# Kernel tuning notes

Measured on AMD Instinct MI355X. Metric: run time of the kernel, lower is better.

The kernel has to match this reference:

```python
import jax, jax.numpy as jnp
import numpy as np

LATENT = 16
HID = 512
N_CLASSES = 10
STYLE = 64
B = 8192


def _he(key, shape, fan_in):
    return jax.random.normal(key, shape, dtype=jnp.float32) * jnp.sqrt(2.0 / fan_in)


def setup_inputs() -> dict:
    key = jax.random.key(0)
    ks = jax.random.split(key, 20)
    inp = {}
    inp['z'] = jax.random.normal(ks[0], (B, LATENT), dtype=jnp.float32)
    inp['y'] = jax.random.randint(ks[1], (B,), 0, N_CLASSES)
    inp['sw0'] = _he(ks[2], (LATENT, HID), LATENT)
    inp['sb0'] = jnp.zeros((HID,), jnp.float32)
    inp['sw1'] = _he(ks[3], (HID, HID), HID)
    inp['sb1'] = jnp.zeros((HID,), jnp.float32)
    inp['sw2'] = _he(ks[4], (HID, HID), HID)
    inp['sb2'] = jnp.zeros((HID,), jnp.float32)
    inp['sw3'] = _he(ks[5], (HID, HID), HID)
    inp['sb3'] = jnp.zeros((HID,), jnp.float32)
    # unshared per-class experts stacked on leading class axis C
    inp['uw0'] = _he(ks[6], (N_CLASSES, HID, HID), HID)
    inp['ub0'] = jnp.zeros((N_CLASSES, HID), jnp.float32)
    inp['uw1'] = _he(ks[7], (N_CLASSES, HID, HID), HID)
    inp['ub1'] = jnp.zeros((N_CLASSES, HID), jnp.float32)
    inp['uw2'] = _he(ks[8], (N_CLASSES, HID, HID), HID)
    inp['ub2'] = jnp.zeros((N_CLASSES, HID), jnp.float32)
    inp['uw3'] = _he(ks[9], (N_CLASSES, HID, STYLE), HID)
    inp['ub3'] = jnp.zeros((N_CLASSES, STYLE), jnp.float32)
    return inp


def reference(z, y, sw0, sb0, sw1, sb1, sw2, sb2, sw3, sb3,
              uw0, ub0, uw1, ub1, uw2, ub2, uw3, ub3):
    # shared trunk: 4 Linear+ReLU
    h = jax.nn.relu(z @ sw0 + sb0)
    h = jax.nn.relu(h @ sw1 + sb1)
    h = jax.nn.relu(h @ sw2 + sb2)
    h = jax.nn.relu(h @ sw3 + sb3)          # [B, H]
    # all per-class expert branches (matches original dense computation)
    o = jax.nn.relu(jnp.einsum('bd,cde->bce', h, uw0) + ub0)   # [B, C, H]
    o = jax.nn.relu(jnp.einsum('bcd,cde->bce', o, uw1) + ub1)
    o = jax.nn.relu(jnp.einsum('bcd,cde->bce', o, uw2) + ub2)
    out = jnp.einsum('bcd,cds->bcs', o, uw3) + ub3             # [B, C, S], no ReLU
    # gather the branch matching each sample's class
    s = out[jnp.arange(out.shape[0]), y]                        # [B, S]
    return s
```

## Files before the change

### kernel.cpp

```cpp
#include <hip/hip_runtime.h>

#define B_SAMPLES 8192
#define HID       512
#define NCLS      10
#define STYLE_D   64
#define LATENT_D  16

#define BM 128
#define BN 64
#define BK 64
#define MAXT    (B_SAMPLES/BM + NCLS)
#define MAXROWS (B_SAMPLES + NCLS*BM)

typedef short v8s __attribute__((ext_vector_type(8)));
typedef float v4f __attribute__((ext_vector_type(4)));

__device__ __forceinline__ short f2bf(float f) {
    union { float f; unsigned u; } x; x.f = f;
    unsigned r = x.u + 0x7fffu + ((x.u >> 16) & 1u);
    return (short)(r >> 16);
}

__device__ __forceinline__ void gload16(const short* g, short* l) {
    __builtin_amdgcn_global_load_lds(
        (const __attribute__((address_space(1))) void*)g,
        (__attribute__((address_space(3))) void*)l, 16, 0, 0);
}

__device__ __forceinline__ int kswz(int row, int k) {
    return (k & ~63) + ((((k >> 3) & 7) ^ (row & 7)) << 3) + (k & 7);
}
__device__ __forceinline__ int cswz(int key, int n0, int c) {
    return n0 + ((((c >> 3) ^ key) & 7) << 3) + (c & 7);
}

__global__ void build_groups(const int* __restrict__ y, int* __restrict__ tclass,
                             int* __restrict__ trow0, int* __restrict__ order,
                             int* __restrict__ rank) {
    __shared__ int cnt[NCLS], cur[NCLS];
    int t = threadIdx.x;
    if (t < NCLS) cnt[t] = 0;
    __syncthreads();
    for (int b = t; b < B_SAMPLES; b += 1024) atomicAdd(&cnt[y[b]], 1);
    __syncthreads();
    if (t == 0) {
        int off = 0, tt = 0;
        for (int c = 0; c < NCLS; ++c) {
            cur[c] = off;
            int nt = (cnt[c] + BM - 1) / BM;
            for (int j = 0; j < nt; ++j) { tclass[tt] = c; trow0[tt] = off + j * BM; ++tt; }
            off += nt * BM;
        }
        for (int u = tt; u < MAXT; ++u) { tclass[u] = -1; trow0[u] = 0; }
    }
    __syncthreads();
    for (int i = t; i < MAXROWS; i += 1024) order[i] = -1;
    __syncthreads();
    for (int b = t; b < B_SAMPLES; b += 1024) {
        int c = y[b];
        int p = atomicAdd(&cur[c], 1);
        order[p] = b;
        rank[b] = p;
    }
}

__global__ void transpose_mega(const float* __restrict__ z,
                               const float* __restrict__ sw0, const float* __restrict__ sw1,
                               const float* __restrict__ sw2, const float* __restrict__ sw3,
                               const float* __restrict__ uw0, const float* __restrict__ uw1,
                               const float* __restrict__ uw2, const float* __restrict__ uw3,
                               short* __restrict__ zb,
                               short* __restrict__ wt0, short* __restrict__ wt1,
                               short* __restrict__ wt2, short* __restrict__ wt3,
                               short* __restrict__ wtu0, short* __restrict__ wtu1,
                               short* __restrict__ wtu2, short* __restrict__ wtu3) {
    __shared__ float tile[32][33];
    int zz = blockIdx.z;
    int tx = threadIdx.x, ty = threadIdx.y;
    if (zz == 35) {
        int t = ty * 32 + tx;
        int base = (blockIdx.y * 20 + blockIdx.x) * 256 + t;
        for (int i = base; i < B_SAMPLES * 64; i += 320 * 256) {
            int b = i >> 6, k = i & 63;
            zb[b * 64 + kswz(b, k)] =
                f2bf(k < LATENT_D ? z[(size_t)b * LATENT_D + k] : 0.f);
        }
        return;
    }
    if (zz == 34) {
        if (blockIdx.x >= 16 || blockIdx.y >= 2) return;
        int n0 = blockIdx.x * 32, k0 = blockIdx.y * 32;
        #pragma unroll
        for (int j = 0; j < 32; j += 8) {
            int k = k0 + ty + j;
            tile[ty + j][tx] = (k < LATENT_D) ? sw0[(size_t)k * HID + n0 + tx] : 0.f;
        }
        __syncthreads();
        #pragma unroll
        for (int j = 0; j < 32; j += 8) {
            int n = n0 + ty + j, k = k0 + tx;
            wt0[n * 64 + kswz(n, k)] = f2bf(tile[tx][ty + j]);
        }
        return;
    }
    if (zz == 33) {
        int cls = blockIdx.x >> 1;
        int n0 = (blockIdx.x & 1) * 32, k0 = blockIdx.y * 32;
        const float* s = uw3  + (size_t)cls * HID * STYLE_D;
        short*       d = wtu3 + (size_t)cls * STYLE_D * HID;
        #pragma unroll
        for (int j = 0; j < 32; j += 8)
            tile[ty + j][tx] = s[(size_t)(k0 + ty + j) * STYLE_D + n0 + tx];
        __syncthreads();
        #pragma unroll
        for (int j = 0; j < 32; j += 8) {
            int n = n0 + ty + j, k = k0 + tx;
            d[(size_t)n * HID + kswz(n, k)] = f2bf(tile[tx][ty + j]);
        }
        return;
    }
    if (blockIdx.x >= 16) return;
    const float* s; short* d;
    if      (zz == 0) { s = sw1; d = wt1; }
    else if (zz == 1) { s = sw2; d = wt2; }
    else if (zz == 2) { s = sw3; d = wt3; }
    else if (zz < 13) { size_t o = (size_t)(zz - 3)  * HID * HID; s = uw0 + o; d = wtu0 + o; }
    else if (zz < 23) { size_t o = (size_t)(zz - 13) * HID * HID; s = uw1 + o; d = wtu1 + o; }
    else              { size_t o = (size_t)(zz - 23) * HID * HID; s = uw2 + o; d = wtu2 + o; }
    int n0 = blockIdx.x * 32, k0 = blockIdx.y * 32;
    #pragma unroll
    for (int j = 0; j < 32; j += 8)
        tile[ty + j][tx] = s[(size_t)(k0 + ty + j) * HID + n0 + tx];
    __syncthreads();
    #pragma unroll
    for (int j = 0; j < 32; j += 8) {
        int n = n0 + ty + j, k = k0 + tx;
        d[(size_t)n * HID + kswz(n, k)] = f2bf(tile[tx][ty + j]);
    }
}

template <int MODE, int NK>
__global__ __launch_bounds__(256, 2) void gemmp(
    const short* __restrict__ A, const short* __restrict__ WT,
    const float* __restrict__ bias, void* __restrict__ Outv,
    const int N, const long wStride, const int biasN,
    const int* __restrict__ aux, const int* __restrict__ tclass,
    const int* __restrict__ trow0) {

    constexpr int K = NK * BK;
    const unsigned gx = gridDim.x;
    const unsigned nwg = gx * gridDim.y;
    unsigned lin = blockIdx.x + gx * blockIdx.y;
    {
        unsigned q = nwg >> 3, r = nwg & 7, xcd = lin & 7, idx = lin >> 3;
        lin = (xcd < r ? xcd * (q + 1) : r * (q + 1) + (xcd - r) * q) + idx;
    }
    const unsigned bx = lin % gx, by = lin / gx;

    int tile = by, cls = 0, row0;
    if (MODE <= 1) {
        row0 = tile * BM;
    } else {
        cls = tclass[tile];
        if (cls < 0) return;
        row0 = trow0[tile];
    }
    const int n0 = bx * BN;
    const short* wt = WT + (size_t)cls * wStride;
    const float* bs = bias + (size_t)cls * biasN;

    __shared__ short As[3][BM * BK];
    __shared__ short Bs[3][BN * BK];

    const int t = threadIdx.x, lane = t & 63, w = t >> 6;
    const int srow = lane >> 3, scol = (lane & 7) * 8;
    const int wr = w >> 1, wc = w & 1;
    const int lrow = lane & 15, lko = lane >> 4;
    const int key = lrow & 7;

    v4f acc[4][2] = {};

    auto stage = [&](int buf, int k0) {
        #pragma unroll
        for (int p = 0; p < 4; ++p) {
            int row = p * 32 + w * 8 + srow;
            gload16(A + (size_t)(row0 + row) * K + k0 + scol, &As[buf][p * 2048 + w * 512]);
        }
        #pragma unroll
        for (int q2 = 0; q2 < 2; ++q2) {
            int row = q2 * 32 + w * 8 + srow;
            gload16(wt + (size_t)(n0 + row) * K + k0 + scol, &Bs[buf][q2 * 2048 + w * 512]);
        }
    };

    stage(0, 0);
    if (NK > 1) stage(1, BK);

    #pragma unroll
    for (int ks = 0; ks < NK; ++ks) {
        const int buf = ks % 3;
        if (ks < NK - 1) asm volatile("s_waitcnt vmcnt(6)" ::: "memory");
        else             asm volatile("s_waitcnt vmcnt(0)" ::: "memory");
        asm volatile("s_barrier" ::: "memory");
        if (ks + 2 < NK) stage((ks + 2) % 3, (ks + 2) * BK);

        __builtin_amdgcn_s_setprio(1);
        #pragma unroll
        for (int kk = 0; kk < 2; ++kk) {
            int ch = ((kk * 4 + lko) ^ key) << 3;
            v8s af[4], bq[2];
            #pragma unroll
            for (int i = 0; i < 4; ++i)
                af[i] = *(const v8s*)&As[buf][(wr * 64 + i * 16 + lrow) * BK + ch];
            #pragma unroll
            for (int j = 0; j < 2; ++j)
                bq[j] = *(const v8s*)&Bs[buf][(wc * 32 + j * 16 + lrow) * BK + ch];
            #pragma unroll
            for (int i = 0; i < 4; ++i)
                #pragma unroll
                for (int j = 0; j < 2; ++j)
                    acc[i][j] = __builtin_amdgcn_mfma_f32_16x16x32_bf16(
                        af[i], bq[j], acc[i][j], 0, 0, 0);
        }
        __builtin_amdgcn_s_setprio(0);
    }

    #pragma unroll
    for (int i = 0; i < 4; ++i)
        #pragma unroll
        for (int j = 0; j < 2; ++j)
            #pragma unroll
            for (int q3 = 0; q3 < 4; ++q3) {
                int rr = wr * 64 + i * 16 + lko * 4 + q3;
                int c = wc * 32 + j * 16 + lrow;
                if (MODE == 3) {
                    int o = aux[row0 + rr];
                    if (o >= 0)
                        ((float*)Outv)[(size_t)o * STYLE_D + n0 + c] = acc[i][j][q3] + bs[n0 + c];
                } else {
                    float v = fmaxf(acc[i][j][q3] + bs[n0 + c], 0.f);
                    int orow = (MODE == 1) ? aux[row0 + rr] : (row0 + rr);
                    ((short*)Outv)[(size_t)orow * N + cswz(orow & 7, n0, c)] = f2bf(v);
                }
            }
}

extern "C" void kernel_launch(void* const* d_in, const int* in_sizes, int n_in,
                              void* d_out, int out_size, void* d_ws, size_t ws_size,
                              hipStream_t stream) {
    const float* z   = (const float*)d_in[0];
    const int*   y   = (const int*)d_in[1];
    const float* sw0 = (const float*)d_in[2];
    const float* sb0 = (const float*)d_in[3];
    const float* sw1 = (const float*)d_in[4];
    const float* sb1 = (const float*)d_in[5];
    const float* sw2 = (const float*)d_in[6];
    const float* sb2 = (const float*)d_in[7];
    const float* sw3 = (const float*)d_in[8];
    const float* sb3 = (const float*)d_in[9];
    const float* uw0 = (const float*)d_in[10];
    const float* ub0 = (const float*)d_in[11];
    const float* uw1 = (const float*)d_in[12];
    const float* ub1 = (const float*)d_in[13];
    const float* uw2 = (const float*)d_in[14];
    const float* ub2 = (const float*)d_in[15];
    const float* uw3 = (const float*)d_in[16];
    const float* ub3 = (const float*)d_in[17];

    char* p = (char*)d_ws;
    auto alloc = [&](size_t bytes) -> char* {
        char* r = p; p += (bytes + 255) & ~(size_t)255; return r;
    };
    int*   tclass = (int*)alloc(MAXT * 4);
    int*   trow0  = (int*)alloc(MAXT * 4);
    int*   order  = (int*)alloc(MAXROWS * 4);
    int*   rank   = (int*)alloc(B_SAMPLES * 4);
    short* zb     = (short*)alloc((size_t)B_SAMPLES * 64 * 2);
    short* wt0    = (short*)alloc((size_t)HID * 64 * 2);
    short* wt1    = (short*)alloc((size_t)HID * HID * 2);
    short* wt2    = (short*)alloc((size_t)HID * HID * 2);
    short* wt3    = (short*)alloc((size_t)HID * HID * 2);
    short* wtu0   = (short*)alloc((size_t)NCLS * HID * HID * 2);
    short* wtu1   = (short*)alloc((size_t)NCLS * HID * HID * 2);
    short* wtu2   = (short*)alloc((size_t)NCLS * HID * HID * 2);
    short* wtu3   = (short*)alloc((size_t)NCLS * STYLE_D * HID * 2);
    short* act0   = (short*)alloc((size_t)MAXROWS * HID * 2);
    short* act1   = (short*)alloc((size_t)MAXROWS * HID * 2);
    short* act2   = (short*)alloc((size_t)MAXROWS * HID * 2);

    build_groups<<<1, 1024, 0, stream>>>(y, tclass, trow0, order, rank);
    dim3 tb(32, 8);
    transpose_mega<<<dim3(20, 16, 36), tb, 0, stream>>>(
        z, sw0, sw1, sw2, sw3, uw0, uw1, uw2, uw3,
        zb, wt0, wt1, wt2, wt3, wtu0, wtu1, wtu2, wtu3);

    gemmp<0, 1><<<dim3(HID / BN, B_SAMPLES / BM), 256, 0, stream>>>(
        zb, wt0, sb0, act0, HID, 0, 0, nullptr, nullptr, nullptr);
    gemmp<0, 8><<<dim3(HID / BN, B_SAMPLES / BM), 256, 0, stream>>>(
        act0, wt1, sb1, act1, HID, 0, 0, nullptr, nullptr, nullptr);
    gemmp<0, 8><<<dim3(HID / BN, B_SAMPLES / BM), 256, 0, stream>>>(
        act1, wt2, sb2, act0, HID, 0, 0, nullptr, nullptr, nullptr);
    gemmp<1, 8><<<dim3(HID / BN, B_SAMPLES / BM), 256, 0, stream>>>(
        act0, wt3, sb3, act2, HID, 0, 0, rank, nullptr, nullptr);

    gemmp<2, 8><<<dim3(HID / BN, MAXT), 256, 0, stream>>>(
        act2, wtu0, ub0, act0, HID, (long)HID * HID, HID, nullptr, tclass, trow0);
    gemmp<2, 8><<<dim3(HID / BN, MAXT), 256, 0, stream>>>(
        act0, wtu1, ub1, act1, HID, (long)HID * HID, HID, nullptr, tclass, trow0);
    gemmp<2, 8><<<dim3(HID / BN, MAXT), 256, 0, stream>>>(
        act1, wtu2, ub2, act0, HID, (long)HID * HID, HID, nullptr, tclass, trow0);
    gemmp<3, 8><<<dim3(1, MAXT), 256, 0, stream>>>(
        act0, wtu3, ub3, d_out, HID, (long)STYLE_D * HID, STYLE_D, order, tclass, trow0);
}
```

Before: 124.9 us.

## Use 8-wave GEMM blocks with double buffering and fuse prep kernels

Each GEMM block now runs 512 threads (8 waves). Each wave computes a 32x32 sub-tile instead of 64x32, and loads are spread across more waves. The 3-stage LDS pipeline with explicit vmcnt waits and setprio is replaced by a simpler 2-stage double buffer synchronized with __syncthreads. The build_groups kernel is folded into the transpose/prep kernel as an extra z-slice to save a launch. The aim is more waves to hide latency, at the cost of less per-wave reuse, a shallower prefetch and heavier barrier traffic.

```diff
diff --git a/kernel.cpp b/kernel.cpp
--- a/kernel.cpp
+++ b/kernel.cpp
@@ -34,51 +34,51 @@
     return n0 + ((((c >> 3) ^ key) & 7) << 3) + (c & 7);
 }
 
-__global__ void build_groups(const int* __restrict__ y, int* __restrict__ tclass,
-                             int* __restrict__ trow0, int* __restrict__ order,
-                             int* __restrict__ rank) {
-    __shared__ int cnt[NCLS], cur[NCLS];
-    int t = threadIdx.x;
-    if (t < NCLS) cnt[t] = 0;
-    __syncthreads();
-    for (int b = t; b < B_SAMPLES; b += 1024) atomicAdd(&cnt[y[b]], 1);
-    __syncthreads();
-    if (t == 0) {
-        int off = 0, tt = 0;
-        for (int c = 0; c < NCLS; ++c) {
-            cur[c] = off;
-            int nt = (cnt[c] + BM - 1) / BM;
-            for (int j = 0; j < nt; ++j) { tclass[tt] = c; trow0[tt] = off + j * BM; ++tt; }
-            off += nt * BM;
-        }
-        for (int u = tt; u < MAXT; ++u) { tclass[u] = -1; trow0[u] = 0; }
-    }
-    __syncthreads();
-    for (int i = t; i < MAXROWS; i += 1024) order[i] = -1;
-    __syncthreads();
-    for (int b = t; b < B_SAMPLES; b += 1024) {
-        int c = y[b];
-        int p = atomicAdd(&cur[c], 1);
-        order[p] = b;
-        rank[b] = p;
-    }
-}
-
-__global__ void transpose_mega(const float* __restrict__ z,
-                               const float* __restrict__ sw0, const float* __restrict__ sw1,
-                               const float* __restrict__ sw2, const float* __restrict__ sw3,
-                               const float* __restrict__ uw0, const float* __restrict__ uw1,
-                               const float* __restrict__ uw2, const float* __restrict__ uw3,
-                               short* __restrict__ zb,
-                               short* __restrict__ wt0, short* __restrict__ wt1,
-                               short* __restrict__ wt2, short* __restrict__ wt3,
-                               short* __restrict__ wtu0, short* __restrict__ wtu1,
-                               short* __restrict__ wtu2, short* __restrict__ wtu3) {
+__global__ void prep_all(const float* __restrict__ z, const int* __restrict__ y,
+                         const float* __restrict__ sw0, const float* __restrict__ sw1,
+                         const float* __restrict__ sw2, const float* __restrict__ sw3,
+                         const float* __restrict__ uw0, const float* __restrict__ uw1,
+                         const float* __restrict__ uw2, const float* __restrict__ uw3,
+                         short* __restrict__ zb,
+                         short* __restrict__ wt0, short* __restrict__ wt1,
+                         short* __restrict__ wt2, short* __restrict__ wt3,
+                         short* __restrict__ wtu0, short* __restrict__ wtu1,
+                         short* __restrict__ wtu2, short* __restrict__ wtu3,
+                         int* __restrict__ tclass, int* __restrict__ trow0,
+                         int* __restrict__ order, int* __restrict__ rank) {
     __shared__ float tile[32][33];
     int zz = blockIdx.z;
     int tx = threadIdx.x, ty = threadIdx.y;
+    int t = ty * 32 + tx;
+    if (zz == 36) {
+        if (blockIdx.x || blockIdx.y) return;
+        __shared__ int cnt[NCLS], cur[NCLS];
+        if (t < NCLS) cnt[t] = 0;
+        __syncthreads();
+        for (int b = t; b < B_SAMPLES; b += 256) atomicAdd(&cnt[y[b]], 1);
+        __syncthreads();
+        if (t == 0) {
+            int off = 0, tt = 0;
+            for (int c = 0; c < NCLS; ++c) {
+                cur[c] = off;
+                int nt = (cnt[c] + BM - 1) / BM;
+                for (int j = 0; j < nt; ++j) { tclass[tt] = c; trow0[tt] = off + j * BM; ++tt; }
+                off += nt * BM;
+            }
+            for (int u = tt; u < MAXT; ++u) { tclass[u] = -1; trow0[u] = 0; }
+        }
+        __syncthreads();
+        for (int i = t; i < MAXROWS; i += 256) order[i] = -1;
+        __syncthreads();
+        for (int b = t; b < B_SAMPLES; b += 256) {
+            int c = y[b];
+            int p = atomicAdd(&cur[c], 1);
+            order[p] = b;
+            rank[b] = p;
+        }
+        return;
+    }
     if (zz == 35) {
-        int t = ty * 32 + tx;
         int base = (blockIdx.y * 20 + blockIdx.x) * 256 + t;
         for (int i = base; i < B_SAMPLES * 64; i += 320 * 256) {
             int b = i >> 6, k = i & 63;
@@ -105,6 +105,7 @@
     }
     if (zz == 33) {
         int cls = blockIdx.x >> 1;
+        if (cls >= NCLS) return;
         int n0 = (blockIdx.x & 1) * 32, k0 = blockIdx.y * 32;
         const float* s = uw3  + (size_t)cls * HID * STYLE_D;
         short*       d = wtu3 + (size_t)cls * STYLE_D * HID;
@@ -140,7 +141,7 @@
 }
 
 template <int MODE, int NK>
-__global__ __launch_bounds__(256, 2) void gemmp(
+__global__ __launch_bounds__(512, 4) void gemm8w(
     const short* __restrict__ A, const short* __restrict__ WT,
     const float* __restrict__ bias, void* __restrict__ Outv,
     const int N, const long wStride, const int biasN,
@@ -169,8 +170,8 @@
     const short* wt = WT + (size_t)cls * wStride;
     const float* bs = bias + (size_t)cls * biasN;
 
-    __shared__ short As[3][BM * BK];
-    __shared__ short Bs[3][BN * BK];
+    __shared__ short As[2][BM * BK];
+    __shared__ short Bs[2][BN * BK];
 
     const int t = threadIdx.x, lane = t & 63, w = t >> 6;
     const int srow = lane >> 3, scol = (lane & 7) * 8;
@@ -178,60 +179,54 @@
     const int lrow = lane & 15, lko = lane >> 4;
     const int key = lrow & 7;
 
-    v4f acc[4][2] = {};
+    v4f acc[2][2] = {};
 
     auto stage = [&](int buf, int k0) {
         #pragma unroll
-        for (int p = 0; p < 4; ++p) {
-            int row = p * 32 + w * 8 + srow;
-            gload16(A + (size_t)(row0 + row) * K + k0 + scol, &As[buf][p * 2048 + w * 512]);
-        }
-        #pragma unroll
-        for (int q2 = 0; q2 < 2; ++q2) {
-            int row = q2 * 32 + w * 8 + srow;
-            gload16(wt + (size_t)(n0 + row) * K + k0 + scol, &Bs[buf][q2 * 2048 + w * 512]);
-        }
+        for (int p = 0; p < 2; ++p) {
+            int row = w * 16 + p * 8 + srow;
+            gload16(A + (size_t)(row0 + row) * K + k0 + scol,
+                    &As[buf][(w * 16 + p * 8) * 64]);
+        }
+        int rowb = w * 8 + srow;
+        gload16(wt + (size_t)(n0 + rowb) * K + k0 + scol,
+                &Bs[buf][(w * 8) * 64]);
     };
 
     stage(0, 0);
-    if (NK > 1) stage(1, BK);
-
+    __syncthreads();
     #pragma unroll
     for (int ks = 0; ks < NK; ++ks) {
-        const int buf = ks % 3;
-        if (ks < NK - 1) asm volatile("s_waitcnt vmcnt(6)" ::: "memory");
-        else             asm volatile("s_waitcnt vmcnt(0)" ::: "memory");
-        asm volatile("s_barrier" ::: "memory");
-        if (ks + 2 < NK) stage((ks + 2) % 3, (ks + 2) * BK);
-
-        __builtin_amdgcn_s_setprio(1);
+        int buf = ks & 1;
+        if (ks + 1 < NK) stage(buf ^ 1, (ks + 1) * BK);
+
         #pragma unroll
         for (int kk = 0; kk < 2; ++kk) {
             int ch = ((kk * 4 + lko) ^ key) << 3;
-            v8s af[4], bq[2];
+            v8s af[2], bq[2];
             #pragma unroll
-            for (int i = 0; i < 4; ++i)
-                af[i] = *(const v8s*)&As[buf][(wr * 64 + i * 16 + lrow) * BK + ch];
+            for (int i = 0; i < 2; ++i)
+                af[i] = *(const v8s*)&As[buf][(wr * 32 + i * 16 + lrow) * BK + ch];
             #pragma unroll
             for (int j = 0; j < 2; ++j)
                 bq[j] = *(const v8s*)&Bs[buf][(wc * 32 + j * 16 + lrow) * BK + ch];
             #pragma unroll
-            for (int i = 0; i < 4; ++i)
+            for (int i = 0; i < 2; ++i)
                 #pragma unroll
                 for (int j = 0; j < 2; ++j)
                     acc[i][j] = __builtin_amdgcn_mfma_f32_16x16x32_bf16(
                         af[i], bq[j], acc[i][j], 0, 0, 0);
         }
-        __builtin_amdgcn_s_setprio(0);
+        __syncthreads();
     }
 
     #pragma unroll
-    for (int i = 0; i < 4; ++i)
+    for (int i = 0; i < 2; ++i)
         #pragma unroll
         for (int j = 0; j < 2; ++j)
             #pragma unroll
             for (int q3 = 0; q3 < 4; ++q3) {
-                int rr = wr * 64 + i * 16 + lko * 4 + q3;
+                int rr = wr * 32 + i * 16 + lko * 4 + q3;
                 int c = wc * 32 + j * 16 + lrow;
                 if (MODE == 3) {
                     int o = aux[row0 + rr];
@@ -288,27 +283,27 @@
     short* act1   = (short*)alloc((size_t)MAXROWS * HID * 2);
     short* act2   = (short*)alloc((size_t)MAXROWS * HID * 2);
 
-    build_groups<<<1, 1024, 0, stream>>>(y, tclass, trow0, order, rank);
     dim3 tb(32, 8);
-    transpose_mega<<<dim3(20, 16, 36), tb, 0, stream>>>(
-        z, sw0, sw1, sw2, sw3, uw0, uw1, uw2, uw3,
-        zb, wt0, wt1, wt2, wt3, wtu0, wtu1, wtu2, wtu3);
-
-    gemmp<0, 1><<<dim3(HID / BN, B_SAMPLES / BM), 256, 0, stream>>>(
+    prep_all<<<dim3(20, 16, 37), tb, 0, stream>>>(
+        z, y, sw0, sw1, sw2, sw3, uw0, uw1, uw2, uw3,
+        zb, wt0, wt1, wt2, wt3, wtu0, wtu1, wtu2, wtu3,
+        tclass, trow0, order, rank);
+
+    gemm8w<0, 1><<<dim3(HID / BN, B_SAMPLES / BM), 512, 0, stream>>>(
         zb, wt0, sb0, act0, HID, 0, 0, nullptr, nullptr, nullptr);
-    gemmp<0, 8><<<dim3(HID / BN, B_SAMPLES / BM), 256, 0, stream>>>(
+    gemm8w<0, 8><<<dim3(HID / BN, B_SAMPLES / BM), 512, 0, stream>>>(
         act0, wt1, sb1, act1, HID, 0, 0, nullptr, nullptr, nullptr);
-    gemmp<0, 8><<<dim3(HID / BN, B_SAMPLES / BM), 256, 0, stream>>>(
+    gemm8w<0, 8><<<dim3(HID / BN, B_SAMPLES / BM), 512, 0, stream>>>(
         act1, wt2, sb2, act0, HID, 0, 0, nullptr, nullptr, nullptr);
-    gemmp<1, 8><<<dim3(HID / BN, B_SAMPLES / BM), 256, 0, stream>>>(
+    gemm8w<1, 8><<<dim3(HID / BN, B_SAMPLES / BM), 512, 0, stream>>>(
         act0, wt3, sb3, act2, HID, 0, 0, rank, nullptr, nullptr);
 
-    gemmp<2, 8><<<dim3(HID / BN, MAXT), 256, 0, stream>>>(
+    gemm8w<2, 8><<<dim3(HID / BN, MAXT), 512, 0, stream>>>(
         act2, wtu0, ub0, act0, HID, (long)HID * HID, HID, nullptr, tclass, trow0);
-    gemmp<2, 8><<<dim3(HID / BN, MAXT), 256, 0, stream>>>(
+    gemm8w<2, 8><<<dim3(HID / BN, MAXT), 512, 0, stream>>>(
         act0, wtu1, ub1, act1, HID, (long)HID * HID, HID, nullptr, tclass, trow0);
-    gemmp<2, 8><<<dim3(HID / BN, MAXT), 256, 0, stream>>>(
+    gemm8w<2, 8><<<dim3(HID / BN, MAXT), 512, 0, stream>>>(
         act1, wtu2, ub2, act0, HID, (long)HID * HID, HID, nullptr, tclass, trow0);
-    gemmp<3, 8><<<dim3(1, MAXT), 256, 0, stream>>>(
+    gemm8w<3, 8><<<dim3(1, MAXT), 512, 0, stream>>>(
         act0, wtu3, ub3, d_out, HID, (long)STYLE_D * HID, STYLE_D, order, tclass, trow0);
 }
```

Result: faster. 117.7 us (-5.8%).
